# Performance work log

Hardware: AMD Instinct MI355X
Metric: run time of the kernel (lower is better)

Reference implementation:

```python
import jax, jax.numpy as jnp
import numpy as np

H = 1024   # hidden_dim
NH = 16    # num_heads
HD = H // NH  # head_dim = 64
B, S = 2, 2048
LN_EPS = 1e-5


def setup_inputs() -> dict:
    key = jax.random.key(0)
    ks = jax.random.split(key, 5)
    scale = 1.0 / np.sqrt(H)  # xavier-ish scale for stability
    return {
        "x": jax.random.normal(ks[0], (B, S, H), dtype=jnp.float32),
        "Wq": jax.random.normal(ks[1], (H, H), dtype=jnp.float32) * scale,
        "bq": jnp.zeros((H,), jnp.float32),
        "Wk": jax.random.normal(ks[2], (H, H), dtype=jnp.float32) * scale,
        "bk": jnp.zeros((H,), jnp.float32),
        "Wv": jax.random.normal(ks[3], (H, H), dtype=jnp.float32) * scale,
        "bv": jnp.zeros((H,), jnp.float32),
        "Wo": jax.random.normal(ks[4], (H, H), dtype=jnp.float32) * scale,
        "bo": jnp.zeros((H,), jnp.float32),
        "ln_gamma": jnp.ones((H,), jnp.float32),
        "ln_beta": jnp.zeros((H,), jnp.float32),
    }


def reference(x, Wq, bq, Wk, bk, Wv, bv, Wo, bo, ln_gamma, ln_beta):
    b, s, _ = x.shape
    # QKV projections, split heads: (b, nh, s, hd)
    def split_heads(t):
        return t.reshape(b, s, NH, HD).transpose(0, 2, 1, 3)
    Q = split_heads(x @ Wq + bq)
    K = split_heads(x @ Wk + bk)
    V = split_heads(x @ Wv + bv)
    # scaled dot-product with clamp (mask=None path)
    scores = jnp.einsum('bhqd,bhkd->bhqk', Q, K) / np.sqrt(HD).astype(np.float32)
    scores = jnp.clip(scores, -10000.0, 10000.0)
    attn = jax.nn.softmax(scores, axis=-1)
    # dropout is identity in eval mode
    ctx = jnp.einsum('bhqk,bhkd->bhqd', attn, V)
    ctx = ctx.transpose(0, 2, 1, 3).reshape(b, s, H)
    out = ctx @ Wo + bo
    # residual + LayerNorm
    y = out + x
    mu = jnp.mean(y, axis=-1, keepdims=True)
    var = jnp.mean(jnp.square(y - mu), axis=-1, keepdims=True)
    y = (y - mu) * jax.lax.rsqrt(var + LN_EPS)
    return y * ln_gamma + ln_beta
```

## Files before the change

kernel.cpp:

```cpp
#include <hip/hip_runtime.h>

typedef unsigned short u16;
typedef __attribute__((ext_vector_type(8))) short shortx8;
typedef __attribute__((ext_vector_type(4))) float floatx4;
typedef __attribute__((ext_vector_type(2))) float floatx2;
typedef __attribute__((ext_vector_type(2))) unsigned uintx2;
typedef __attribute__((ext_vector_type(4))) unsigned uintx4;

#define GLD16(gp, lp) __builtin_amdgcn_global_load_lds( \
    (__attribute__((address_space(1))) void*)(gp), \
    (__attribute__((address_space(3))) void*)(lp), 16, 0, 0)

__device__ __forceinline__ u16 f2bf(float f) {
  union { float f; unsigned u; } v; v.f = f;
  unsigned r = v.u + 0x7FFFu + ((v.u >> 16) & 1u);
  return (u16)(r >> 16);
}

__device__ __forceinline__ unsigned pkbf(float a, float b) {
#if __has_builtin(__builtin_amdgcn_cvt_pk_bf16_f32)
  auto r = __builtin_amdgcn_cvt_pk_bf16_f32(a, b);
  return __builtin_bit_cast(unsigned, r);
#else
  union { float f; unsigned u; } x, y; x.f = a; y.f = b;
  return __builtin_amdgcn_perm(y.u + 0x8000u, x.u + 0x8000u, 0x07060302u);
#endif
}

__global__ __launch_bounds__(256) void prep_kernel(const float* __restrict__ x,
                                                   u16* __restrict__ xb,
                                                   const float* __restrict__ Wq,
                                                   const float* __restrict__ Wk,
                                                   const float* __restrict__ Wv,
                                                   const float* __restrict__ Wo,
                                                   u16* __restrict__ Wt) {
  __shared__ u16 tile[32][33];
  int bid = blockIdx.x;
  int tid = threadIdx.x;
  if (bid < 4096) {
    int i = bid * 256 + tid;
    float4 v = ((const float4*)x)[i];
    uintx2 o;
    o.x = pkbf(v.x, v.y);
    o.y = pkbf(v.z, v.w);
    ((uintx2*)xb)[i] = o;
  } else {
    int block = bid - 4096;
    int mat = block >> 10;
    int rem = block & 1023;
    const float* W = (mat == 0) ? Wq : (mat == 1) ? Wk : (mat == 2) ? Wv : Wo;
    u16* dst = Wt + (size_t)mat * 1024 * 1024;
    int n0 = (rem & 31) * 32, k0 = (rem >> 5) * 32;
    int tx = tid & 31, ty = tid >> 5;
    for (int i = 0; i < 4; ++i)
      tile[ty + i * 8][tx] = f2bf(W[(size_t)(k0 + ty + i * 8) * 1024 + n0 + tx]);
    __syncthreads();
    for (int i = 0; i < 4; ++i)
      dst[(size_t)(n0 + ty + i * 8) * 1024 + k0 + tx] = tile[tx][ty + i * 8];
  }
}

__device__ __forceinline__ void gemm_tile_core(const u16* __restrict__ A,
                                               const u16* __restrict__ Bt,
                                               int m0, int n0,
                                               u16* As, u16* Bs,
                                               floatx4 (&acc)[4][4]) {
  const int tid = threadIdx.x;
  const int wave = tid >> 6, lane = tid & 63;
  const int lrow = lane >> 4, lcol = lane & 15;
  const int wm = wave >> 1, wn = wave & 1;

  for (int mi = 0; mi < 4; ++mi)
    for (int ni = 0; ni < 4; ++ni)
      acc[mi][ni] = (floatx4){0.f, 0.f, 0.f, 0.f};

  const u16* ap[4];
  const u16* bp[4];
  for (int l = 0; l < 4; ++l) {
    int g = (l * 4 + wave) * 64 + lane;
    int r = g >> 3, c = g & 7;
    int cc = (c ^ (r & 7)) * 8;
    ap[l] = A + (size_t)(m0 + r) * 1024 + cc;
    bp[l] = Bt + (size_t)(n0 + r) * 1024 + cc;
  }

  for (int k0 = 0; k0 < 1024; k0 += 64) {
    __syncthreads();
    for (int l = 0; l < 4; ++l) {
      GLD16(ap[l], As + (l * 4 + wave) * 512);
      GLD16(bp[l], Bs + (l * 4 + wave) * 512);
      ap[l] += 64; bp[l] += 64;
    }
    __syncthreads();
    for (int kk = 0; kk < 2; ++kk) {
      shortx8 af[4], bf[4];
      for (int mi = 0; mi < 4; ++mi) {
        int row = wm * 64 + mi * 16 + lcol;
        int gr = (kk * 4 + lrow) ^ (row & 7);
        af[mi] = *(const shortx8*)&As[row * 64 + gr * 8];
      }
      for (int ni = 0; ni < 4; ++ni) {
        int row = wn * 64 + ni * 16 + lcol;
        int gr = (kk * 4 + lrow) ^ (row & 7);
        bf[ni] = *(const shortx8*)&Bs[row * 64 + gr * 8];
      }
      for (int mi = 0; mi < 4; ++mi)
        for (int ni = 0; ni < 4; ++ni)
          acc[mi][ni] = __builtin_amdgcn_mfma_f32_16x16x32_bf16(af[mi], bf[ni], acc[mi][ni], 0, 0, 0);
    }
  }
}

__global__ __launch_bounds__(256) void qkv_gemm(const u16* __restrict__ xb,
                                                const u16* __restrict__ Wt,
                                                const float* __restrict__ bq,
                                                const float* __restrict__ bk,
                                                const float* __restrict__ bv,
                                                u16* __restrict__ Qh,
                                                u16* __restrict__ Kh,
                                                u16* __restrict__ Vth) {
  __shared__ u16 sbuf[128 * 128];
  u16* As = sbuf;
  u16* Bs = sbuf + 128 * 64;
  int m0 = blockIdx.x * 128;
  int mat = blockIdx.y >> 3;
  int n0 = (blockIdx.y & 7) * 128;
  floatx4 acc[4][4];
  gemm_tile_core(xb, Wt + (size_t)mat * 1024 * 1024, m0, n0, As, Bs, acc);

  const float* bias = (mat == 0) ? bq : (mat == 1) ? bk : bv;
  const int tid = threadIdx.x;
  const int wave = tid >> 6, lane = tid & 63;
  const int lrow = lane >> 4, lcol = lane & 15;
  const int wm = wave >> 1, wn = wave & 1;
  const float qscale = 0.18033688011f;

  if (mat < 2) {
    u16* dst = (mat == 0) ? Qh : Kh;
    float sc = (mat == 0) ? qscale : 1.0f;
    __syncthreads();
    for (int mi = 0; mi < 4; ++mi) {
      int mb = wm * 64 + mi * 16 + lrow * 4;
      for (int ni = 0; ni < 4; ++ni) {
        int n = wn * 64 + ni * 16 + lcol;
        float bval = bias[n0 + n];
        for (int r = 0; r < 4; ++r) {
          int m = mb + r;
          sbuf[m * 128 + (((n >> 3) ^ (m & 15)) * 8) + (n & 7)] =
              f2bf((acc[mi][ni][r] + bval) * sc);
        }
      }
    }
    __syncthreads();
    int row = tid >> 1, half = tid & 1;
    int m = m0 + row;
    int bb = m >> 11, s = m & 2047;
    for (int i = 0; i < 8; ++i) {
      int cg = half * 8 + i;
      int pg = cg ^ (row & 15);
      shortx8 v = *(const shortx8*)&sbuf[row * 128 + pg * 8];
      int ng = n0 + cg * 8;
      int h = ng >> 6, d = ng & 63;
      *(shortx8*)&dst[((size_t)(bb * 16 + h) * 2048 + s) * 64 + d] = v;
    }
  } else {
    for (int mi = 0; mi < 4; ++mi) {
      int mbase = m0 + wm * 64 + mi * 16 + lrow * 4;
      int bb = mbase >> 11, s = mbase & 2047;
      for (int ni = 0; ni < 4; ++ni) {
        int n = n0 + wn * 64 + ni * 16 + lcol;
        float bval = bias[n];
        int h = n >> 6, d = n & 63;
        uintx2 pk;
        pk.x = pkbf(acc[mi][ni][0] + bval, acc[mi][ni][1] + bval);
        pk.y = pkbf(acc[mi][ni][2] + bval, acc[mi][ni][3] + bval);
        *(uintx2*)&Vth[((size_t)(bb * 16 + h) * 64 + d) * 2048 + s] = pk;
      }
    }
  }
}

__global__ __launch_bounds__(256) void out_gemm(const u16* __restrict__ ctx,
                                                const u16* __restrict__ Wot,
                                                const float* __restrict__ bo,
                                                float* __restrict__ aout) {
  __shared__ u16 As[128 * 64];
  __shared__ u16 Bs[64 * 64];
  int m0 = blockIdx.x * 128;
  int n0 = blockIdx.y * 64;
  const int tid = threadIdx.x;
  const int wave = tid >> 6, lane = tid & 63;
  const int lrow = lane >> 4, lcol = lane & 15;
  const int wm = wave >> 1, wn = wave & 1;

  floatx4 acc[4][2];
  for (int mi = 0; mi < 4; ++mi)
    for (int ni = 0; ni < 2; ++ni)
      acc[mi][ni] = (floatx4){0.f, 0.f, 0.f, 0.f};

  const u16* ap[4];
  const u16* bp[2];
  for (int l = 0; l < 4; ++l) {
    int g = (l * 4 + wave) * 64 + lane;
    int r = g >> 3, c = g & 7;
    ap[l] = ctx + (size_t)(m0 + r) * 1024 + (c ^ (r & 7)) * 8;
  }
  for (int l = 0; l < 2; ++l) {
    int g = (l * 4 + wave) * 64 + lane;
    int r = g >> 3, c = g & 7;
    bp[l] = Wot + (size_t)(n0 + r) * 1024 + (c ^ (r & 7)) * 8;
  }

  for (int k0 = 0; k0 < 1024; k0 += 64) {
    __syncthreads();
    for (int l = 0; l < 4; ++l) { GLD16(ap[l], As + (l * 4 + wave) * 512); ap[l] += 64; }
    for (int l = 0; l < 2; ++l) { GLD16(bp[l], Bs + (l * 4 + wave) * 512); bp[l] += 64; }
    __syncthreads();
    for (int kk = 0; kk < 2; ++kk) {
      shortx8 af[4], bf[2];
      for (int mi = 0; mi < 4; ++mi) {
        int row = wm * 64 + mi * 16 + lcol;
        int gr = (kk * 4 + lrow) ^ (row & 7);
        af[mi] = *(const shortx8*)&As[row * 64 + gr * 8];
      }
      for (int ni = 0; ni < 2; ++ni) {
        int row = wn * 32 + ni * 16 + lcol;
        int gr = (kk * 4 + lrow) ^ (row & 7);
        bf[ni] = *(const shortx8*)&Bs[row * 64 + gr * 8];
      }
      for (int mi = 0; mi < 4; ++mi)
        for (int ni = 0; ni < 2; ++ni)
          acc[mi][ni] = __builtin_amdgcn_mfma_f32_16x16x32_bf16(af[mi], bf[ni], acc[mi][ni], 0, 0, 0);
    }
  }

  for (int mi = 0; mi < 4; ++mi) {
    int mbase = m0 + wm * 64 + mi * 16 + lrow * 4;
    for (int ni = 0; ni < 2; ++ni) {
      int n = n0 + wn * 32 + ni * 16 + lcol;
      float bval = bo[n];
      for (int r = 0; r < 4; ++r)
        aout[(size_t)(mbase + r) * 1024 + n] = acc[mi][ni][r] + bval;
    }
  }
}

__global__ __launch_bounds__(512) void attn_kernel(const u16* __restrict__ Qh,
                                                   const u16* __restrict__ Kh,
                                                   const u16* __restrict__ Vth,
                                                   u16* __restrict__ ctx) {
  __shared__ u16 QPs[128 * 64];
  __shared__ u16 Ks[2][64 * 64];
  __shared__ u16 Vs[2][64 * 64];

  int bh = blockIdx.x;
  int b = bh >> 4, h = bh & 15;
  int q0 = blockIdx.y * 128;
  int tid = threadIdx.x;
  int wave = tid >> 6, lane = tid & 63;
  int lrow = lane >> 4, lcol = lane & 15;

  const u16* Qg = Qh + ((size_t)bh * 2048 + q0) * 64;
  for (int l = 0; l < 2; ++l) {
    int g = (l * 8 + wave) * 64 + lane;
    int r = g >> 3, c = g & 7;
    GLD16(Qg + r * 64 + ((c ^ (r & 7)) * 8), QPs + (l * 8 + wave) * 512);
  }

  const u16* Kbase = Kh + (size_t)bh * 2048 * 64;
  const u16* Vbase = Vth + (size_t)bh * 64 * 2048;

  int g = wave * 64 + lane;
  int gr = g >> 3, gc = g & 7;
  int cc = (gc ^ (gr & 7)) * 8;
  const u16* kp = Kbase + (size_t)gr * 64 + cc;

  const u16* vp = Vbase + (size_t)gr * 2048 + gc * 8;
  int hh = gc >> 2, ct = gc & 3;
  int ua = 4 * (ct & 1) + (ct >> 1);
  int chunkA = hh * 4 + (ua >> 1);
  int offA = gr * 128 + ((chunkA ^ (gr & 7)) * 16) + (ua & 1) * 8;
  int offB = gr * 128 + (((chunkA + 1) ^ (gr & 7)) * 16) + (ua & 1) * 8;

  {
    float4 vreg = *(const float4*)vp;
    vp += 64;
    GLD16(kp, (u16*)Ks + wave * 512);
    kp += 4096;
    char* vb = (char*)Vs;
    *(floatx2*)(vb + offA) = (floatx2){vreg.x, vreg.y};
    *(floatx2*)(vb + offB) = (floatx2){vreg.z, vreg.w};
  }
  __syncthreads();

  shortx8 qf[2];
  for (int kk = 0; kk < 2; ++kk) {
    int row = wave * 16 + lcol;
    int grr = (kk * 4 + lrow) ^ (row & 7);
    qf[kk] = *(const shortx8*)&QPs[row * 64 + grr * 8];
  }

  const short one_bf = (short)0x3F80;
  const shortx8 ones8 = {one_bf, one_bf, one_bf, one_bf, one_bf, one_bf, one_bf, one_bf};

  floatx4 o[4];
  floatx4 lacc = (floatx4){0.f, 0.f, 0.f, 0.f};
  for (int dt = 0; dt < 4; ++dt) o[dt] = (floatx4){0.f, 0.f, 0.f, 0.f};

  for (int i = 0; i < 32; ++i) {
    int cur = i & 1;
    float4 vreg;
    if (i < 31) {
      vreg = *(const float4*)vp;
      vp += 64;
      GLD16(kp, (u16*)Ks + (cur ^ 1) * 4096 + wave * 512);
      kp += 4096;
    }

    floatx4 sc[4];
    for (int kt = 0; kt < 4; ++kt)
      sc[kt] = (floatx4){0.f, 0.f, 0.f, 0.f};
    __builtin_amdgcn_s_setprio(1);
    for (int kk = 0; kk < 2; ++kk) {
      for (int kt = 0; kt < 4; ++kt) {
        int row = kt * 16 + lcol;
        int grr = (kk * 4 + lrow) ^ (row & 7);
        shortx8 kf = *(const shortx8*)&Ks[cur][row * 64 + grr * 8];
        sc[kt] = __builtin_amdgcn_mfma_f32_16x16x32_bf16(kf, qf[kk], sc[kt], 0, 0, 0);
      }
    }
    __builtin_amdgcn_s_setprio(0);

    float p[4][4];
    for (int kt = 0; kt < 4; ++kt)
      for (int r = 0; r < 4; ++r)
        p[kt][r] = __builtin_amdgcn_exp2f(sc[kt][r]);
    shortx8 pf[2];
    for (int kk = 0; kk < 2; ++kk) {
      uintx4 w;
      w.x = pkbf(p[2 * kk][0], p[2 * kk][1]);
      w.y = pkbf(p[2 * kk][2], p[2 * kk][3]);
      w.z = pkbf(p[2 * kk + 1][0], p[2 * kk + 1][1]);
      w.w = pkbf(p[2 * kk + 1][2], p[2 * kk + 1][3]);
      pf[kk] = __builtin_bit_cast(shortx8, w);
    }

    if (i < 31) {
      char* vb = (char*)Vs + (cur ^ 1) * 8192;
      *(floatx2*)(vb + offA) = (floatx2){vreg.x, vreg.y};
      *(floatx2*)(vb + offB) = (floatx2){vreg.z, vreg.w};
    }

    __builtin_amdgcn_s_setprio(1);
    for (int kk = 0; kk < 2; ++kk) {
      lacc = __builtin_amdgcn_mfma_f32_16x16x32_bf16(ones8, pf[kk], lacc, 0, 0, 0);
      for (int dt = 0; dt < 4; ++dt) {
        int row = dt * 16 + lcol;
        int grr = (kk * 4 + lrow) ^ (row & 7);
        shortx8 vf = *(const shortx8*)&Vs[cur][row * 64 + grr * 8];
        o[dt] = __builtin_amdgcn_mfma_f32_16x16x32_bf16(vf, pf[kk], o[dt], 0, 0, 0);
      }
    }
    __builtin_amdgcn_s_setprio(0);
    __syncthreads();
  }

  {
    float inv = 1.0f / lacc[0];
    int s = q0 + wave * 16 + lcol;
    u16* dst = ctx + (size_t)(b * 2048 + s) * 1024 + h * 64 + lrow * 4;
    for (int dt = 0; dt < 4; ++dt) {
      uintx2 pk;
      pk.x = pkbf(o[dt][0] * inv, o[dt][1] * inv);
      pk.y = pkbf(o[dt][2] * inv, o[dt][3] * inv);
      *(uintx2*)(dst + dt * 16) = pk;
    }
  }
}

__global__ __launch_bounds__(256) void ln_kernel(const float* __restrict__ aout,
                                                 const float* __restrict__ x,
                                                 const float* __restrict__ gamma,
                                                 const float* __restrict__ beta,
                                                 float* __restrict__ out) {
  int row = blockIdx.x;
  int t = threadIdx.x;
  const float4* a4 = (const float4*)(aout + (size_t)row * 1024);
  const float4* x4 = (const float4*)(x + (size_t)row * 1024);
  float4 v = a4[t];
  float4 xv = x4[t];
  v.x += xv.x; v.y += xv.y; v.z += xv.z; v.w += xv.w;
  float s = v.x + v.y + v.z + v.w;
  float s2 = v.x * v.x + v.y * v.y + v.z * v.z + v.w * v.w;
  for (int off = 1; off < 64; off <<= 1) {
    s += __shfl_xor(s, off, 64);
    s2 += __shfl_xor(s2, off, 64);
  }
  __shared__ float red[8];
  int wave = t >> 6, lane = t & 63;
  if (lane == 0) { red[wave] = s; red[4 + wave] = s2; }
  __syncthreads();
  s = red[0] + red[1] + red[2] + red[3];
  s2 = red[4] + red[5] + red[6] + red[7];
  float mu = s * (1.0f / 1024.0f);
  float var = s2 * (1.0f / 1024.0f) - mu * mu;
  float rstd = rsqrtf(var + 1e-5f);
  float4 g = ((const float4*)gamma)[t];
  float4 be = ((const float4*)beta)[t];
  float4 y;
  y.x = (v.x - mu) * rstd * g.x + be.x;
  y.y = (v.y - mu) * rstd * g.y + be.y;
  y.z = (v.z - mu) * rstd * g.z + be.z;
  y.w = (v.w - mu) * rstd * g.w + be.w;
  ((float4*)(out + (size_t)row * 1024))[t] = y;
}

extern "C" void kernel_launch(void* const* d_in, const int* in_sizes, int n_in,
                              void* d_out, int out_size, void* d_ws, size_t ws_size,
                              hipStream_t stream) {
  const float* x     = (const float*)d_in[0];
  const float* Wq    = (const float*)d_in[1];
  const float* bq    = (const float*)d_in[2];
  const float* Wk    = (const float*)d_in[3];
  const float* bk    = (const float*)d_in[4];
  const float* Wv    = (const float*)d_in[5];
  const float* bv    = (const float*)d_in[6];
  const float* Wo    = (const float*)d_in[7];
  const float* bo    = (const float*)d_in[8];
  const float* gamma = (const float*)d_in[9];
  const float* beta  = (const float*)d_in[10];
  float* out = (float*)d_out;

  char* ws = (char*)d_ws;
  u16* xb   = (u16*)(ws);
  u16* Wt   = (u16*)(ws + ((size_t)8 << 20));
  u16* Qh   = (u16*)(ws + ((size_t)16 << 20));
  u16* Kh   = (u16*)(ws + ((size_t)24 << 20));
  u16* Vth  = (u16*)(ws + ((size_t)32 << 20));
  u16* ctx  = (u16*)(ws + ((size_t)40 << 20));
  float* aout = (float*)(ws + ((size_t)48 << 20));

  prep_kernel<<<8192, 256, 0, stream>>>(x, xb, Wq, Wk, Wv, Wo, Wt);
  qkv_gemm<<<dim3(32, 24), 256, 0, stream>>>(xb, Wt, bq, bk, bv, Qh, Kh, Vth);
  attn_kernel<<<dim3(32, 16), 512, 0, stream>>>(Qh, Kh, Vth, ctx);
  out_gemm<<<dim3(32, 16), 256, 0, stream>>>(ctx, Wt + (size_t)3 * 1024 * 1024, bo, aout);
  ln_kernel<<<4096, 256, 0, stream>>>(aout, x, gamma, beta, out);
}
```

Baseline: 204.3 us.

## Rewrite QKV GEMM as 256x256 tile with double-buffered LDS pipeline

The QKV projection GEMM moves from 128x128 tiles with 4 waves to 256x256 tiles with 8 waves. The K loop now double-buffers the LDS tiles and overlaps the next tile's global-to-LDS loads with MFMA work, using explicit barriers, waitcnts and setprio around each MFMA chunk. The aim is to hide global load latency and raise data reuse per block. In exchange it uses 128KB of LDS and many accumulator registers, and the grid shrinks to 192 blocks, which may underfill the 256 CUs.

```diff
diff --git a/kernel.cpp b/kernel.cpp
--- a/kernel.cpp
+++ b/kernel.cpp
@@ -10,6 +10,12 @@
 #define GLD16(gp, lp) __builtin_amdgcn_global_load_lds( \
     (__attribute__((address_space(1))) void*)(gp), \
     (__attribute__((address_space(3))) void*)(lp), 16, 0, 0)
+
+#define BAR() __builtin_amdgcn_s_barrier()
+#define LGKM0() do { asm volatile("s_waitcnt lgkmcnt(0)" ::: "memory"); \
+                     __builtin_amdgcn_sched_barrier(0); } while (0)
+#define VMCNT0() do { asm volatile("s_waitcnt vmcnt(0)" ::: "memory"); \
+                      __builtin_amdgcn_sched_barrier(0); } while (0)
 
 __device__ __forceinline__ u16 f2bf(float f) {
   union { float f; unsigned u; } v; v.f = f;
@@ -60,93 +66,174 @@
   }
 }
 
-__device__ __forceinline__ void gemm_tile_core(const u16* __restrict__ A,
-                                               const u16* __restrict__ Bt,
-                                               int m0, int n0,
-                                               u16* As, u16* Bs,
-                                               floatx4 (&acc)[4][4]) {
+template <int MIB>
+__device__ __forceinline__ void qkv_lda(const u16* Ah, int lrow, int lcol,
+                                        shortx8 (&afr)[2][2]) {
+#pragma unroll
+  for (int j = 0; j < 2; ++j) {
+    int rm = (MIB + j) * 16 + lcol;
+#pragma unroll
+    for (int kk = 0; kk < 2; ++kk)
+      afr[j][kk] = *(const shortx8*)&Ah[rm * 64 + (((kk * 4 + lrow) ^ (rm & 7)) * 8)];
+  }
+}
+
+template <int MIB>
+__device__ __forceinline__ void qkv_mfma(floatx4 (&acc)[8][4],
+                                         const shortx8 (&afr)[2][2],
+                                         const shortx8 (&bfr)[4][2]) {
+#pragma unroll
+  for (int kk = 0; kk < 2; ++kk)
+#pragma unroll
+    for (int j = 0; j < 2; ++j)
+#pragma unroll
+      for (int ni = 0; ni < 4; ++ni)
+        acc[MIB + j][ni] = __builtin_amdgcn_mfma_f32_16x16x32_bf16(
+            afr[j][kk], bfr[ni][kk], acc[MIB + j][ni], 0, 0, 0);
+}
+
+__global__ __launch_bounds__(512, 2) void qkv_gemm(const u16* __restrict__ xb,
+                                                   const u16* __restrict__ Wt,
+                                                   const float* __restrict__ bq,
+                                                   const float* __restrict__ bk,
+                                                   const float* __restrict__ bv,
+                                                   u16* __restrict__ Qh,
+                                                   u16* __restrict__ Kh,
+                                                   u16* __restrict__ Vth) {
+  __shared__ u16 lds[65536];
   const int tid = threadIdx.x;
   const int wave = tid >> 6, lane = tid & 63;
   const int lrow = lane >> 4, lcol = lane & 15;
-  const int wm = wave >> 1, wn = wave & 1;
-
-  for (int mi = 0; mi < 4; ++mi)
+  const int wm = wave >> 2, wn = wave & 3;
+  const int m0 = blockIdx.x * 256;
+  const int nt = blockIdx.y;
+  const int mat = nt >> 2;
+  const int n0 = (nt & 3) * 256;
+  const u16* Ag = xb;
+  const u16* Bg = Wt + (size_t)mat * 1048576;
+
+  const u16* sa[2][2];
+  const u16* sb[2][2];
+#pragma unroll
+  for (int h = 0; h < 2; ++h)
+#pragma unroll
+    for (int l = 0; l < 2; ++l) {
+      int g = (l * 8 + wave) * 64 + lane;
+      int r = g >> 3, c = g & 7;
+      int cc = (c ^ (r & 7)) * 8;
+      sa[h][l] = Ag + (size_t)(m0 + h * 128 + r) * 1024 + cc;
+      sb[h][l] = Bg + (size_t)(n0 + h * 128 + r) * 1024 + cc;
+    }
+
+  floatx4 acc[8][4];
+#pragma unroll
+  for (int mi = 0; mi < 8; ++mi)
+#pragma unroll
     for (int ni = 0; ni < 4; ++ni)
       acc[mi][ni] = (floatx4){0.f, 0.f, 0.f, 0.f};
 
-  const u16* ap[4];
-  const u16* bp[4];
-  for (int l = 0; l < 4; ++l) {
-    int g = (l * 4 + wave) * 64 + lane;
-    int r = g >> 3, c = g & 7;
-    int cc = (c ^ (r & 7)) * 8;
-    ap[l] = A + (size_t)(m0 + r) * 1024 + cc;
-    bp[l] = Bt + (size_t)(n0 + r) * 1024 + cc;
-  }
-
-  for (int k0 = 0; k0 < 1024; k0 += 64) {
-    __syncthreads();
-    for (int l = 0; l < 4; ++l) {
-      GLD16(ap[l], As + (l * 4 + wave) * 512);
-      GLD16(bp[l], Bs + (l * 4 + wave) * 512);
-      ap[l] += 64; bp[l] += 64;
-    }
-    __syncthreads();
-    for (int kk = 0; kk < 2; ++kk) {
-      shortx8 af[4], bf[4];
-      for (int mi = 0; mi < 4; ++mi) {
-        int row = wm * 64 + mi * 16 + lcol;
-        int gr = (kk * 4 + lrow) ^ (row & 7);
-        af[mi] = *(const shortx8*)&As[row * 64 + gr * 8];
-      }
-      for (int ni = 0; ni < 4; ++ni) {
-        int row = wn * 64 + ni * 16 + lcol;
-        int gr = (kk * 4 + lrow) ^ (row & 7);
-        bf[ni] = *(const shortx8*)&Bs[row * 64 + gr * 8];
-      }
-      for (int mi = 0; mi < 4; ++mi)
-        for (int ni = 0; ni < 4; ++ni)
-          acc[mi][ni] = __builtin_amdgcn_mfma_f32_16x16x32_bf16(af[mi], bf[ni], acc[mi][ni], 0, 0, 0);
-    }
-  }
-}
-
-__global__ __launch_bounds__(256) void qkv_gemm(const u16* __restrict__ xb,
-                                                const u16* __restrict__ Wt,
-                                                const float* __restrict__ bq,
-                                                const float* __restrict__ bk,
-                                                const float* __restrict__ bv,
-                                                u16* __restrict__ Qh,
-                                                u16* __restrict__ Kh,
-                                                u16* __restrict__ Vth) {
-  __shared__ u16 sbuf[128 * 128];
-  u16* As = sbuf;
-  u16* Bs = sbuf + 128 * 64;
-  int m0 = blockIdx.x * 128;
-  int mat = blockIdx.y >> 3;
-  int n0 = (blockIdx.y & 7) * 128;
-  floatx4 acc[4][4];
-  gemm_tile_core(xb, Wt + (size_t)mat * 1024 * 1024, m0, n0, As, Bs, acc);
+#pragma unroll
+  for (int h = 0; h < 2; ++h)
+#pragma unroll
+    for (int l = 0; l < 2; ++l) {
+      GLD16(sa[h][l], lds + h * 8192 + (l * 8 + wave) * 512);
+      GLD16(sb[h][l], lds + 16384 + h * 8192 + (l * 8 + wave) * 512);
+    }
+  VMCNT0();
+  BAR();
+
+#pragma unroll 2
+  for (int t = 0; t < 16; ++t) {
+    const int rb = t & 1, wb = rb ^ 1;
+    const u16* Ah = lds + rb * 32768 + wm * 8192;
+    const u16* Bh = lds + rb * 32768 + 16384 + (wn >> 1) * 8192;
+    u16* Aw = lds + wb * 32768;
+    u16* Bw = lds + wb * 32768 + 16384;
+
+    if (t < 15) {
+      int k64 = (t + 1) * 64;
+#pragma unroll
+      for (int l = 0; l < 2; ++l) {
+        GLD16(sa[0][l] + k64, Aw + (l * 8 + wave) * 512);
+        GLD16(sa[1][l] + k64, Aw + 8192 + (l * 8 + wave) * 512);
+      }
+    }
+    shortx8 bfr[4][2];
+#pragma unroll
+    for (int ni = 0; ni < 4; ++ni) {
+      int rn = (wn & 1) * 64 + ni * 16 + lcol;
+#pragma unroll
+      for (int kk = 0; kk < 2; ++kk)
+        bfr[ni][kk] = *(const shortx8*)&Bh[rn * 64 + (((kk * 4 + lrow) ^ (rn & 7)) * 8)];
+    }
+    {
+      shortx8 afr[2][2];
+      qkv_lda<0>(Ah, lrow, lcol, afr);
+      BAR();
+      LGKM0();
+      __builtin_amdgcn_s_setprio(1);
+      qkv_mfma<0>(acc, afr, bfr);
+      __builtin_amdgcn_s_setprio(0);
+      BAR();
+    }
+    if (t < 15) {
+      int k64 = (t + 1) * 64;
+#pragma unroll
+      for (int l = 0; l < 2; ++l) {
+        GLD16(sb[0][l] + k64, Bw + (l * 8 + wave) * 512);
+        GLD16(sb[1][l] + k64, Bw + 8192 + (l * 8 + wave) * 512);
+      }
+    }
+    {
+      shortx8 afr[2][2];
+      qkv_lda<2>(Ah, lrow, lcol, afr);
+      BAR();
+      LGKM0();
+      __builtin_amdgcn_s_setprio(1);
+      qkv_mfma<2>(acc, afr, bfr);
+      __builtin_amdgcn_s_setprio(0);
+      BAR();
+    }
+    {
+      shortx8 afr[2][2];
+      qkv_lda<4>(Ah, lrow, lcol, afr);
+      BAR();
+      LGKM0();
+      __builtin_amdgcn_s_setprio(1);
+      qkv_mfma<4>(acc, afr, bfr);
+      __builtin_amdgcn_s_setprio(0);
+      BAR();
+    }
+    {
+      shortx8 afr[2][2];
+      qkv_lda<6>(Ah, lrow, lcol, afr);
+      BAR();
+      LGKM0();
+      __builtin_amdgcn_s_setprio(1);
+      qkv_mfma<6>(acc, afr, bfr);
+      __builtin_amdgcn_s_setprio(0);
+      VMCNT0();
+      BAR();
+    }
+  }
 
   const float* bias = (mat == 0) ? bq : (mat == 1) ? bk : bv;
-  const int tid = threadIdx.x;
-  const int wave = tid >> 6, lane = tid & 63;
-  const int lrow = lane >> 4, lcol = lane & 15;
-  const int wm = wave >> 1, wn = wave & 1;
   const float qscale = 0.18033688011f;
 
   if (mat < 2) {
     u16* dst = (mat == 0) ? Qh : Kh;
     float sc = (mat == 0) ? qscale : 1.0f;
-    __syncthreads();
-    for (int mi = 0; mi < 4; ++mi) {
-      int mb = wm * 64 + mi * 16 + lrow * 4;
+#pragma unroll
+    for (int mi = 0; mi < 8; ++mi) {
+      int mb = wm * 128 + mi * 16 + lrow * 4;
+#pragma unroll
       for (int ni = 0; ni < 4; ++ni) {
         int n = wn * 64 + ni * 16 + lcol;
         float bval = bias[n0 + n];
+#pragma unroll
         for (int r = 0; r < 4; ++r) {
           int m = mb + r;
-          sbuf[m * 128 + (((n >> 3) ^ (m & 15)) * 8) + (n & 7)] =
+          lds[m * 256 + (((n >> 3) ^ (m & 31)) * 8) + (n & 7)] =
               f2bf((acc[mi][ni][r] + bval) * sc);
         }
       }
@@ -155,26 +242,29 @@
     int row = tid >> 1, half = tid & 1;
     int m = m0 + row;
     int bb = m >> 11, s = m & 2047;
-    for (int i = 0; i < 8; ++i) {
-      int cg = half * 8 + i;
-      int pg = cg ^ (row & 15);
-      shortx8 v = *(const shortx8*)&sbuf[row * 128 + pg * 8];
+#pragma unroll
+    for (int i = 0; i < 16; ++i) {
+      int cg = half * 16 + i;
+      int pg = cg ^ (row & 31);
+      shortx8 v = *(const shortx8*)&lds[row * 256 + pg * 8];
       int ng = n0 + cg * 8;
-      int h = ng >> 6, d = ng & 63;
-      *(shortx8*)&dst[((size_t)(bb * 16 + h) * 2048 + s) * 64 + d] = v;
+      int hh = ng >> 6, d = ng & 63;
+      *(shortx8*)&dst[((size_t)(bb * 16 + hh) * 2048 + s) * 64 + d] = v;
     }
   } else {
-    for (int mi = 0; mi < 4; ++mi) {
-      int mbase = m0 + wm * 64 + mi * 16 + lrow * 4;
+#pragma unroll
+    for (int mi = 0; mi < 8; ++mi) {
+      int mbase = m0 + wm * 128 + mi * 16 + lrow * 4;
       int bb = mbase >> 11, s = mbase & 2047;
+#pragma unroll
       for (int ni = 0; ni < 4; ++ni) {
         int n = n0 + wn * 64 + ni * 16 + lcol;
         float bval = bias[n];
-        int h = n >> 6, d = n & 63;
+        int hh = n >> 6, d = n & 63;
         uintx2 pk;
         pk.x = pkbf(acc[mi][ni][0] + bval, acc[mi][ni][1] + bval);
         pk.y = pkbf(acc[mi][ni][2] + bval, acc[mi][ni][3] + bval);
-        *(uintx2*)&Vth[((size_t)(bb * 16 + h) * 64 + d) * 2048 + s] = pk;
+        *(uintx2*)&Vth[((size_t)(bb * 16 + hh) * 64 + d) * 2048 + s] = pk;
       }
     }
   }
@@ -441,7 +531,7 @@
   float* aout = (float*)(ws + ((size_t)48 << 20));
 
   prep_kernel<<<8192, 256, 0, stream>>>(x, xb, Wq, Wk, Wv, Wo, Wt);
-  qkv_gemm<<<dim3(32, 24), 256, 0, stream>>>(xb, Wt, bq, bk, bv, Qh, Kh, Vth);
+  qkv_gemm<<<dim3(16, 12), 512, 0, stream>>>(xb, Wt, bq, bk, bv, Qh, Kh, Vth);
   attn_kernel<<<dim3(32, 16), 512, 0, stream>>>(Qh, Kh, Vth, ctx);
   out_gemm<<<dim3(32, 16), 256, 0, stream>>>(ctx, Wt + (size_t)3 * 1024 * 1024, bo, aout);
   ln_kernel<<<4096, 256, 0, stream>>>(aout, x, gamma, beta, out);
```

After: 193.6 us. -5.2%, faster.
